# Performance work log

Measured on AMD Instinct MI355X. Metric: run time of the kernel, lower is better.

The kernel has to match this reference:

```python
import jax, jax.numpy as jnp
import numpy as np

NEG_SLOPE = 0.2  # PyG GATConv default


def gat_layer(x, W, a_src, a_dst, b, src, dst, N, H, C):
    # x: [N, F_in]; W: [F_in, H*C]; a_src/a_dst: [H, C]; b: [H*C]
    h = (x @ W).reshape(N, H, C)                      # [N,H,C]
    e_src = jnp.sum(h * a_src, axis=-1)               # [N,H]
    e_dst = jnp.sum(h * a_dst, axis=-1)               # [N,H]
    e = jax.nn.leaky_relu(e_src[src] + e_dst[dst], NEG_SLOPE)  # [E,H]
    # segment softmax over incoming edges of each destination node
    m = jax.ops.segment_max(e, dst, num_segments=N)   # [N,H]
    m = jnp.where(jnp.isfinite(m), m, 0.0)
    p = jnp.exp(e - m[dst])                           # [E,H]
    s = jax.ops.segment_sum(p, dst, num_segments=N)   # [N,H]
    alpha = p / (s[dst] + 1e-16)                      # [E,H]
    msg = alpha[:, :, None] * h[src]                  # [E,H,C]
    out = jax.ops.segment_sum(msg, dst, num_segments=N)  # [N,H,C]
    return out.reshape(N, H * C) + b


def setup_inputs() -> dict:
    key = jax.random.key(0)
    ks = jax.random.split(key, 12)
    N, E, G = 100000, 2000000, 64
    hidden, heads = 32, 4
    x = jax.random.normal(ks[0], (N, 1), dtype=jnp.float32)
    edge_index = jax.random.randint(ks[1], (2, E), 0, N, dtype=jnp.int64)
    batch = jnp.sort(jax.random.randint(ks[2], (N,), 0, G, dtype=jnp.int64))
    s = 0.1
    W1 = jax.random.normal(ks[3], (1, heads * hidden), jnp.float32) * s
    a_src1 = jax.random.normal(ks[4], (heads, hidden), jnp.float32) * s
    a_dst1 = jax.random.normal(ks[5], (heads, hidden), jnp.float32) * s
    b1 = jnp.zeros((heads * hidden,), jnp.float32)
    W2 = jax.random.normal(ks[6], (heads * hidden, hidden), jnp.float32) * s
    a_src2 = jax.random.normal(ks[7], (1, hidden), jnp.float32) * s
    a_dst2 = jax.random.normal(ks[8], (1, hidden), jnp.float32) * s
    b2 = jnp.zeros((hidden,), jnp.float32)
    lin_w = jax.random.normal(ks[9], (hidden, 1), jnp.float32) * s
    lin_b = jnp.zeros((1,), jnp.float32)
    return {"x": x, "edge_index": edge_index, "batch": batch, "num_graphs": G,
            "W1": W1, "a_src1": a_src1, "a_dst1": a_dst1, "b1": b1,
            "W2": W2, "a_src2": a_src2, "a_dst2": a_dst2, "b2": b2,
            "lin_w": lin_w, "lin_b": lin_b}


def reference(x, edge_index, batch, num_graphs, W1, a_src1, a_dst1, b1,
              W2, a_src2, a_dst2, b2, lin_w, lin_b):
    N = x.shape[0]
    hidden, heads = 32, 4
    # PyG GATConv adds self-loops by default
    loops = jnp.arange(N, dtype=edge_index.dtype)
    src = jnp.concatenate([edge_index[0], loops])
    dst = jnp.concatenate([edge_index[1], loops])
    x1 = jax.nn.relu(gat_layer(x, W1, a_src1, a_dst1, b1, src, dst, N, heads, hidden))
    x2 = jax.nn.relu(gat_layer(x1, W2, a_src2, a_dst2, b2, src, dst, N, 1, hidden))
    # global mean pool over graphs
    sums = jax.ops.segment_sum(x2, batch, num_segments=num_graphs)      # [G,hidden]
    cnts = jax.ops.segment_sum(jnp.ones((N,), x2.dtype), batch, num_segments=num_graphs)
    pooled = sums / jnp.maximum(cnts, 1.0)[:, None]
    return jax.nn.sigmoid(pooled @ lin_w + lin_b).squeeze(-1)           # [G]
```

## Files before the change

### kernel.cpp

```cpp
#include <hip/hip_runtime.h>
#include <hip/hip_bf16.h>

#define LRELU(v) ((v) > 0.0f ? (v) : 0.2f * (v))
#define PPARTS 32
#define LCAP 4096
#define BCAP 4096

typedef float f32x2 __attribute__((ext_vector_type(2)));

__device__ __forceinline__ unsigned short f2bf(float f) {
    unsigned int u = __float_as_uint(f);
    unsigned int r = (u >> 16) & 1;
    u += 0x7fff + r;
    return (unsigned short)(u >> 16);
}
__device__ __forceinline__ float bf2f(unsigned short s) {
    return __uint_as_float(((unsigned int)s) << 16);
}

__global__ void k_init(int* __restrict__ cursor, int nb,
                       const float* __restrict__ W1, const float* __restrict__ a1s,
                       const float* __restrict__ a1d, float* __restrict__ dots) {
    int t = threadIdx.x;
    if (t < 128) {
        float w = W1[t];
        float ps = w * a1s[t];
        float pd = w * a1d[t];
        #pragma unroll
        for (int o = 16; o; o >>= 1) {
            ps += __shfl_xor(ps, o, 32);
            pd += __shfl_xor(pd, o, 32);
        }
        if ((t & 31) == 0) {
            dots[t >> 5] = ps;
            dots[4 + (t >> 5)] = pd;
        }
    }
    if (t < nb) cursor[t] = 0;
}

__global__ void k_scat(const int* __restrict__ ei, int* __restrict__ cursor,
                       int* __restrict__ pairbuf, int E, int N, int nb) {
    __shared__ int h[1024];
    __shared__ int basearr[1024];
    int t = threadIdx.x;
    for (int i = t; i < nb; i += 512) h[i] = 0;
    __syncthreads();
    int ET = E + N;
    int base = blockIdx.x * 4096;
    int end = base + 4096 < ET ? base + 4096 : ET;
    for (int e = base + t; e < end; e += 512) {
        int d = (e < E) ? ei[E + e] : (e - E);
        atomicAdd(&h[d >> 7], 1);
    }
    __syncthreads();
    for (int i = t; i < nb; i += 512) {
        int c = h[i];
        basearr[i] = c ? (i * BCAP + atomicAdd(&cursor[i], c)) : 0;
        h[i] = 0;
    }
    __syncthreads();
    for (int e = base + t; e < end; e += 512) {
        int s, d;
        if (e < E) { s = ei[e]; d = ei[E + e]; } else { s = d = e - E; }
        int b = d >> 7;
        int pos = basearr[b] + atomicAdd(&h[b], 1);
        pairbuf[pos] = (s << 7) | (d & 127);
    }
}

__global__ void k_build(const int* __restrict__ pairbuf, const int* __restrict__ cursor,
                        int* __restrict__ rowp, int* __restrict__ degarr, int* __restrict__ col,
                        const float* __restrict__ x, const float* __restrict__ dots,
                        float* __restrict__ S, int N) {
    int b = blockIdx.x;
    __shared__ int deg[128];
    __shared__ int inc[128];
    __shared__ int rbase[128];
    __shared__ int cur[128];
    __shared__ int lcol[LCAP];
    int s0 = b * BCAP;
    int cnt = cursor[b];
    int s1 = s0 + cnt;
    bool uselds = (cnt <= LCAP);
    if (threadIdx.x < 128) deg[threadIdx.x] = 0;
    __syncthreads();
    for (int i = s0 + threadIdx.x; i < s1; i += 512)
        atomicAdd(&deg[pairbuf[i] & 127], 1);
    __syncthreads();
    if (threadIdx.x < 128) {
        int lane = threadIdx.x & 63;
        int sv = deg[threadIdx.x];
        #pragma unroll
        for (int o = 1; o < 64; o <<= 1) {
            int u = __shfl_up(sv, o, 64);
            if (lane >= o) sv += u;
        }
        inc[threadIdx.x] = sv;
    }
    __syncthreads();
    if (threadIdx.x < 128) {
        int excl = inc[threadIdx.x] - deg[threadIdx.x] + ((threadIdx.x >= 64) ? inc[63] : 0);
        rbase[threadIdx.x] = s0 + excl;
        cur[threadIdx.x] = 0;
        int node = (b << 7) + threadIdx.x;
        if (node < N) {
            rowp[node] = s0 + excl;
            degarr[node] = deg[threadIdx.x];
        }
    }
    __syncthreads();
    for (int i = s0 + threadIdx.x; i < s1; i += 512) {
        int p = pairbuf[i];
        int off = p & 127;
        int pos = rbase[off] + atomicAdd(&cur[off], 1);
        int srcn = p >> 7;
        col[pos] = srcn;
        if (uselds) lcol[pos - s0] = srcn;
    }
    __syncthreads();

    float ds0 = dots[0], ds1 = dots[1], ds2 = dots[2], ds3 = dots[3];
    float dd0 = dots[4], dd1 = dots[5], dd2 = dots[6], dd3 = dots[7];
    int lane = threadIdx.x & 15;
    int nl = threadIdx.x >> 4;
    #pragma unroll
    for (int pass = 0; pass < 4; ++pass) {
        int nloc = nl + (pass << 5);
        int node = (b << 7) + nloc;
        if (node >= N) continue;
        int gstart = rbase[nloc];
        int lstart = gstart - s0;
        int dg = deg[nloc];
        float xd = x[node];
        float t0 = xd * dd0, t1 = xd * dd1, t2 = xd * dd2, t3 = xd * dd3;
        float p0 = 0.f, p1 = 0.f, p2 = 0.f, p3 = 0.f;
        float q0 = 0.f, q1 = 0.f, q2 = 0.f, q3 = 0.f;
        for (int i = lane; i < dg; i += 16) {
            int srcn = uselds ? lcol[lstart + i] : col[gstart + i];
            float xs = x[srcn];
            float e0 = LRELU(fmaf(xs, ds0, t0)); float w0 = __expf(e0); p0 += w0; q0 = fmaf(w0, xs, q0);
            float e1 = LRELU(fmaf(xs, ds1, t1)); float w1 = __expf(e1); p1 += w1; q1 = fmaf(w1, xs, q1);
            float e2 = LRELU(fmaf(xs, ds2, t2)); float w2 = __expf(e2); p2 += w2; q2 = fmaf(w2, xs, q2);
            float e3 = LRELU(fmaf(xs, ds3, t3)); float w3 = __expf(e3); p3 += w3; q3 = fmaf(w3, xs, q3);
        }
        #pragma unroll
        for (int o = 8; o; o >>= 1) {
            p0 += __shfl_xor(p0, o, 16); p1 += __shfl_xor(p1, o, 16);
            p2 += __shfl_xor(p2, o, 16); p3 += __shfl_xor(p3, o, 16);
            q0 += __shfl_xor(q0, o, 16); q1 += __shfl_xor(q1, o, 16);
            q2 += __shfl_xor(q2, o, 16); q3 += __shfl_xor(q3, o, 16);
        }
        if (lane == 0) {
            float4 r;
            r.x = q0 / (p0 + 1e-16f);
            r.y = q1 / (p1 + 1e-16f);
            r.z = q2 / (p2 + 1e-16f);
            r.w = q3 / (p3 + 1e-16f);
            *(float4*)(S + node * 4) = r;
        }
    }
}

__global__ void k_h2(const float* __restrict__ S, const float* __restrict__ W1,
                     const float* __restrict__ b1, const float* __restrict__ W2,
                     const float* __restrict__ a2s, const float* __restrict__ a2d,
                     unsigned int* __restrict__ h2f8, float* __restrict__ es2,
                     float* __restrict__ ed2, int N) {
    __shared__ float sW2[4096];
    __shared__ float sW1[128];
    __shared__ float sb1[128];
    for (int i = threadIdx.x; i < 4096; i += blockDim.x) sW2[i] = W2[i];
    if (threadIdx.x < 128) {
        sW1[threadIdx.x] = W1[threadIdx.x];
        sb1[threadIdx.x] = b1[threadIdx.x];
    }
    __syncthreads();
    int n = blockIdx.x * blockDim.x + threadIdx.x;
    if (n >= N) return;
    float4 sv = *(const float4*)(S + (size_t)n * 4);
    float acc[32];
    #pragma unroll
    for (int c = 0; c < 32; ++c) acc[c] = 0.f;
    #pragma unroll
    for (int h = 0; h < 4; ++h) {
        float sh = (h == 0) ? sv.x : (h == 1) ? sv.y : (h == 2) ? sv.z : sv.w;
        for (int cc = 0; cc < 32; ++cc) {
            int hc = h * 32 + cc;
            float x1 = fmaf(sh, sW1[hc], sb1[hc]);
            x1 = x1 > 0.f ? x1 : 0.f;
            const float* w2row = &sW2[hc * 32];
            #pragma unroll
            for (int c = 0; c < 32; ++c) acc[c] = fmaf(x1, w2row[c], acc[c]);
        }
    }
    float es = 0.f, edv = 0.f;
    #pragma unroll
    for (int c = 0; c < 32; ++c) {
        es = fmaf(acc[c], a2s[c], es);
        edv = fmaf(acc[c], a2d[c], edv);
    }
    alignas(16) unsigned int hw[8];
    #pragma unroll
    for (int q = 0; q < 8; ++q) {
        int w = __builtin_amdgcn_cvt_pk_fp8_f32(acc[4 * q + 0], acc[4 * q + 1], 0, false);
        w = __builtin_amdgcn_cvt_pk_fp8_f32(acc[4 * q + 2], acc[4 * q + 3], w, true);
        hw[q] = (unsigned int)w;
    }
    uint4* dst = (uint4*)(h2f8 + (size_t)n * 8);
    dst[0] = ((const uint4*)hw)[0];
    dst[1] = ((const uint4*)hw)[1];
    es2[n] = es;
    ed2[n] = edv;
}

__global__ void k_agg(const unsigned int* __restrict__ h2f8, const float* __restrict__ es2,
                      const float* __restrict__ ed2, const int* __restrict__ rowp,
                      const int* __restrict__ degarr, const int* __restrict__ col,
                      const float* __restrict__ b2, unsigned short* __restrict__ x2buf, int N) {
    int gid = blockIdx.x * blockDim.x + threadIdx.x;
    int n = gid >> 3;
    int lane = threadIdx.x & 7;
    if (n >= N) return;
    int s = rowp[n];
    int deg = degarr[n];
    float ed = ed2[n];
    int slot = lane >> 2;
    int cg = lane & 3;
    float sump = 0.f;
    float a0 = 0.f, a1 = 0.f, a2 = 0.f, a3 = 0.f, a4 = 0.f, a5 = 0.f, a6 = 0.f, a7 = 0.f;
    #pragma unroll 4
    for (int j = slot; j < deg; j += 2) {
        int sidx = col[s + j];
        float e = LRELU(es2[sidx] + ed);
        float p = __expf(e);
        sump += p;
        uint2 hv = *(const uint2*)(h2f8 + (size_t)sidx * 8 + cg * 2);
        f32x2 c01 = __builtin_amdgcn_cvt_pk_f32_fp8((int)hv.x, false);
        f32x2 c23 = __builtin_amdgcn_cvt_pk_f32_fp8((int)hv.x, true);
        f32x2 c45 = __builtin_amdgcn_cvt_pk_f32_fp8((int)hv.y, false);
        f32x2 c67 = __builtin_amdgcn_cvt_pk_f32_fp8((int)hv.y, true);
        a0 = fmaf(p, c01.x, a0); a1 = fmaf(p, c01.y, a1);
        a2 = fmaf(p, c23.x, a2); a3 = fmaf(p, c23.y, a3);
        a4 = fmaf(p, c45.x, a4); a5 = fmaf(p, c45.y, a5);
        a6 = fmaf(p, c67.x, a6); a7 = fmaf(p, c67.y, a7);
    }
    sump += __shfl_xor(sump, 4, 8);
    a0 += __shfl_xor(a0, 4, 8); a1 += __shfl_xor(a1, 4, 8);
    a2 += __shfl_xor(a2, 4, 8); a3 += __shfl_xor(a3, 4, 8);
    a4 += __shfl_xor(a4, 4, 8); a5 += __shfl_xor(a5, 4, 8);
    a6 += __shfl_xor(a6, 4, 8); a7 += __shfl_xor(a7, 4, 8);
    if (slot == 0) {
        float inv = 1.0f / (sump + 1e-16f);
        const float* bb = b2 + cg * 8;
        float v[8] = {a0, a1, a2, a3, a4, a5, a6, a7};
        unsigned int w[4];
        #pragma unroll
        for (int q = 0; q < 4; ++q) {
            float t0 = fmaf(v[2 * q], inv, bb[2 * q]);
            t0 = t0 > 0.f ? t0 : 0.f;
            float t1 = fmaf(v[2 * q + 1], inv, bb[2 * q + 1]);
            t1 = t1 > 0.f ? t1 : 0.f;
            w[q] = (unsigned int)f2bf(t0) | ((unsigned int)f2bf(t1) << 16);
        }
        uint4* dst = (uint4*)(x2buf + (size_t)n * 32 + cg * 8);
        *dst = make_uint4(w[0], w[1], w[2], w[3]);
    }
}

__global__ void k_psum(const unsigned short* __restrict__ x2buf, const int* __restrict__ batch,
                       float* __restrict__ partial, int N) {
    int g = blockIdx.x / PPARTS;
    int part = blockIdx.x % PPARTS;
    __shared__ int sr[2];
    if (threadIdx.x == 0) {
        int lo = 0, hi = N;
        while (lo < hi) { int mid = (lo + hi) >> 1; if (batch[mid] < g) lo = mid + 1; else hi = mid; }
        sr[0] = lo;
        int l2 = lo, h2v = N;
        while (l2 < h2v) { int mid = (l2 + h2v) >> 1; if (batch[mid] < g + 1) l2 = mid + 1; else h2v = mid; }
        sr[1] = l2;
    }
    __syncthreads();
    int lo = sr[0], hi = sr[1];
    int cs = (hi - lo + PPARTS - 1) / PPARTS;
    int start = lo + part * cs;
    int end = start + cs < hi ? start + cs : hi;
    int ch = threadIdx.x & 31;
    int slot = threadIdx.x >> 5;
    float acc = 0.f;
    for (int n = start + slot; n < end; n += 8)
        acc += bf2f(x2buf[(size_t)n * 32 + ch]);
    __shared__ float red[256];
    red[threadIdx.x] = acc;
    __syncthreads();
    #pragma unroll
    for (int o = 128; o >= 32; o >>= 1) {
        if (threadIdx.x < o) red[threadIdx.x] += red[threadIdx.x + o];
        __syncthreads();
    }
    if (threadIdx.x < 32)
        partial[(size_t)(g * PPARTS + part) * 32 + threadIdx.x] = red[threadIdx.x];
}

__global__ void k_head(const float* __restrict__ partial, const int* __restrict__ batch,
                       const float* __restrict__ lin_w, const float* __restrict__ lin_b,
                       float* __restrict__ out, int N) {
    int g = blockIdx.x;
    int t = threadIdx.x;
    int ch = t & 31;
    int half = t >> 5;
    float acc = 0.f;
    for (int p = half * (PPARTS / 2); p < (half + 1) * (PPARTS / 2); ++p)
        acc += partial[(size_t)(g * PPARTS + p) * 32 + ch];
    acc += __shfl_xor(acc, 32, 64);
    int lo = 0, hi = N;
    while (lo < hi) { int mid = (lo + hi) >> 1; if (batch[mid] < g) lo = mid + 1; else hi = mid; }
    int l2 = lo, h2v = N;
    while (l2 < h2v) { int mid = (l2 + h2v) >> 1; if (batch[mid] < g + 1) l2 = mid + 1; else h2v = mid; }
    float c = fmaxf((float)(h2v - lo), 1.0f);
    float v = acc / c * lin_w[ch];
    #pragma unroll
    for (int o = 16; o; o >>= 1) v += __shfl_xor(v, o, 32);
    if (t == 0) out[g] = 1.0f / (1.0f + __expf(-(v + lin_b[0])));
}

extern "C" void kernel_launch(void* const* d_in, const int* in_sizes, int n_in,
                              void* d_out, int out_size, void* d_ws, size_t ws_size,
                              hipStream_t stream) {
    const float* x     = (const float*)d_in[0];
    const int*   ei    = (const int*)d_in[1];
    const int*   batch = (const int*)d_in[2];
    const float* W1    = (const float*)d_in[4];
    const float* a1s   = (const float*)d_in[5];
    const float* a1d   = (const float*)d_in[6];
    const float* b1    = (const float*)d_in[7];
    const float* W2    = (const float*)d_in[8];
    const float* a2s   = (const float*)d_in[9];
    const float* a2d   = (const float*)d_in[10];
    const float* b2    = (const float*)d_in[11];
    const float* lin_w = (const float*)d_in[12];
    const float* lin_b = (const float*)d_in[13];
    float* out = (float*)d_out;

    int N = in_sizes[0];
    int E = in_sizes[1] / 2;
    int ET = E + N;
    int G = out_size;
    int nb = (N + 127) >> 7;
    int nblk = (ET + 4095) / 4096;

    char* ws = (char*)d_ws;
    size_t off = 0;
    auto alloc = [&](size_t bytes) -> char* {
        char* p = ws + off;
        off = (off + bytes + 255) & ~(size_t)255;
        return p;
    };
    int*   cursor  = (int*)alloc(1024 * 4);
    int*   pairbuf = (int*)alloc((size_t)nb * BCAP * 4);
    int*   rowp    = (int*)alloc((size_t)N * 4);
    int*   degarr  = (int*)alloc((size_t)N * 4);
    int*   col     = (int*)alloc((size_t)nb * BCAP * 4);
    float* S       = (float*)alloc((size_t)N * 16);
    unsigned int* h2f8 = (unsigned int*)alloc((size_t)N * 32);
    float* es2     = (float*)alloc((size_t)N * 4);
    float* ed2     = (float*)alloc((size_t)N * 4);
    float* dots    = (float*)alloc(32);
    unsigned short* x2buf = (unsigned short*)alloc((size_t)N * 64);
    float* partial = (float*)alloc((size_t)G * PPARTS * 32 * 4);

    k_init<<<1, 1024, 0, stream>>>(cursor, nb, W1, a1s, a1d, dots);
    k_scat<<<nblk, 512, 0, stream>>>(ei, cursor, pairbuf, E, N, nb);
    k_build<<<nb, 512, 0, stream>>>(pairbuf, cursor, rowp, degarr, col, x, dots, S, N);
    k_h2<<<(N + 255) / 256, 256, 0, stream>>>(S, W1, b1, W2, a2s, a2d, h2f8, es2, ed2, N);
    k_agg<<<((size_t)N * 8 + 255) / 256, 256, 0, stream>>>(h2f8, es2, ed2, rowp, degarr, col, b2, x2buf, N);
    k_psum<<<G * PPARTS, 256, 0, stream>>>(x2buf, batch, partial, N);
    k_head<<<G, 64, 0, stream>>>(partial, batch, lin_w, lin_b, out, N);
}
```

Before: 133.5 us.

## Stage scatter pairs in LDS sorted by bucket before coalesced global write

The edge scatter kernel now sorts each block's edges into shared memory by destination bucket, using a block-wide prefix scan of the bucket histogram. It then writes them out to the global pair buffer in bucket order, so consecutive threads write contiguous runs instead of random single-int scatters. Blocks grow to 1024 threads handling 8192 edges each, which cuts the number of global cursor atomics per bucket. This costs about 58KB of LDS per block, which limits occupancy, and adds extra barriers. It also assumes nb is at most 1024, which holds for N=100000.

Result: faster. 123.3 us (-7.7%).

```diff
diff --git a/kernel.cpp b/kernel.cpp
--- a/kernel.cpp
+++ b/kernel.cpp
@@ -42,30 +42,61 @@
 __global__ void k_scat(const int* __restrict__ ei, int* __restrict__ cursor,
                        int* __restrict__ pairbuf, int E, int N, int nb) {
     __shared__ int h[1024];
+    __shared__ int loff[1024];
     __shared__ int basearr[1024];
+    __shared__ int lpair[8192];
+    __shared__ unsigned short lbid[8192];
+    __shared__ int wsum[16];
     int t = threadIdx.x;
-    for (int i = t; i < nb; i += 512) h[i] = 0;
+    h[t] = 0;
     __syncthreads();
     int ET = E + N;
-    int base = blockIdx.x * 4096;
-    int end = base + 4096 < ET ? base + 4096 : ET;
-    for (int e = base + t; e < end; e += 512) {
+    int base = blockIdx.x * 8192;
+    int end = base + 8192 < ET ? base + 8192 : ET;
+    for (int e = base + t; e < end; e += 1024) {
         int d = (e < E) ? ei[E + e] : (e - E);
         atomicAdd(&h[d >> 7], 1);
     }
     __syncthreads();
-    for (int i = t; i < nb; i += 512) {
-        int c = h[i];
-        basearr[i] = c ? (i * BCAP + atomicAdd(&cursor[i], c)) : 0;
-        h[i] = 0;
-    }
-    __syncthreads();
-    for (int e = base + t; e < end; e += 512) {
+    int v = h[t];
+    int lane = t & 63, w = t >> 6;
+    int sv = v;
+    #pragma unroll
+    for (int o = 1; o < 64; o <<= 1) {
+        int u = __shfl_up(sv, o, 64);
+        if (lane >= o) sv += u;
+    }
+    if (lane == 63) wsum[w] = sv;
+    __syncthreads();
+    if (t < 16) {
+        int ws2 = wsum[t];
+        #pragma unroll
+        for (int o = 1; o < 16; o <<= 1) {
+            int u = __shfl_up(ws2, o, 16);
+            if (t >= o) ws2 += u;
+        }
+        wsum[t] = ws2;
+    }
+    __syncthreads();
+    int excl = sv - v + (w ? wsum[w - 1] : 0);
+    loff[t] = excl;
+    if (t < nb && v) basearr[t] = t * BCAP + atomicAdd(&cursor[t], v);
+    __syncthreads();
+    h[t] = 0;
+    __syncthreads();
+    for (int e = base + t; e < end; e += 1024) {
         int s, d;
         if (e < E) { s = ei[e]; d = ei[E + e]; } else { s = d = e - E; }
         int b = d >> 7;
-        int pos = basearr[b] + atomicAdd(&h[b], 1);
-        pairbuf[pos] = (s << 7) | (d & 127);
+        int lpos = loff[b] + atomicAdd(&h[b], 1);
+        lpair[lpos] = (s << 7) | (d & 127);
+        lbid[lpos] = (unsigned short)b;
+    }
+    __syncthreads();
+    int total = end - base;
+    for (int i = t; i < total; i += 1024) {
+        int b = lbid[i];
+        pairbuf[basearr[b] + (i - loff[b])] = lpair[i];
     }
 }
 
@@ -348,7 +379,7 @@
     int ET = E + N;
     int G = out_size;
     int nb = (N + 127) >> 7;
-    int nblk = (ET + 4095) / 4096;
+    int nblk = (ET + 8191) / 8192;
 
     char* ws = (char*)d_ws;
     size_t off = 0;
@@ -371,7 +402,7 @@
     float* partial = (float*)alloc((size_t)G * PPARTS * 32 * 4);
 
     k_init<<<1, 1024, 0, stream>>>(cursor, nb, W1, a1s, a1d, dots);
-    k_scat<<<nblk, 512, 0, stream>>>(ei, cursor, pairbuf, E, N, nb);
+    k_scat<<<nblk, 1024, 0, stream>>>(ei, cursor, pairbuf, E, N, nb);
     k_build<<<nb, 512, 0, stream>>>(pairbuf, cursor, rowp, degarr, col, x, dots, S, N);
     k_h2<<<(N + 255) / 256, 256, 0, stream>>>(S, W1, b1, W2, a2s, a2d, h2f8, es2, ed2, N);
     k_agg<<<((size_t)N * 8 + 255) / 256, 256, 0, stream>>>(h2f8, es2, ed2, rowp, degarr, col, b2, x2buf, N);
```
